# Kernel optimization log

Hardware: AMD Instinct MI355X
Metric: run time of the kernel (lower is better)

## Reference

```python
import jax, jax.numpy as jnp
import numpy as np

L, B, T, D, H, F = 6, 4, 1024, 512, 8, 2048
DH = D // H
BIAS_DIM = 2
E = 65536
EPS = 1e-3  # LayerNormalization default epsilon in the source


def _ln(x, scale, bias):
    m = jnp.mean(x, axis=-1, keepdims=True)
    v = jnp.mean(jnp.square(x - m), axis=-1, keepdims=True)  # tf.nn.moments: population variance
    return (x - m) * jax.lax.rsqrt(v + EPS) * scale + bias


def setup_inputs() -> dict:
    key = jax.random.key(0)
    ks = jax.random.split(key, 24)
    g = lambda k, shape: (jax.random.normal(k, shape, jnp.float32) * (shape[-1] ** -0.5))
    states = jax.random.normal(ks[0], (B, T, D), jnp.float32)
    # causal mask broadcast over heads: [B, 1, Tq, Tk]
    masks = jnp.tril(jnp.ones((T, T), jnp.float32))[None, None] * jnp.ones((B, 1, 1, 1), jnp.float32)
    # sparse bias edges: columns (edge_type, batch_idx, key_idx, query_idx)
    et = jax.random.randint(ks[1], (E, 1), 0, BIAS_DIM)
    bi = jax.random.randint(ks[2], (E, 1), 0, B)
    ki = jax.random.randint(ks[3], (E, 1), 0, T)
    qi = jax.random.randint(ks[4], (E, 1), 0, T)
    attention_bias = jnp.concatenate([et, bi, ki, qi], axis=1).astype(jnp.int32)
    return dict(
        states=states,
        masks=masks,
        attention_bias=attention_bias,
        Wq=g(ks[5], (L, D, H, DH)),
        Wk=g(ks[6], (L, D, H, DH)),
        Wv=g(ks[7], (L, D, H, DH)),
        Wo=g(ks[8], (L, H, DH, D)),
        Eb=g(ks[9], (L, BIAS_DIM, DH)),
        Es=g(ks[10], (L, DH)),
        ln1_s=jnp.ones((L, D), jnp.float32),
        ln1_b=jnp.zeros((L, D), jnp.float32),
        ln2_s=jnp.ones((L, D), jnp.float32),
        ln2_b=jnp.zeros((L, D), jnp.float32),
        lno_s=jnp.ones((D,), jnp.float32),
        lno_b=jnp.zeros((D,), jnp.float32),
        W1=g(ks[11], (L, D, F)),
        b1=jnp.zeros((L, F), jnp.float32),
        W2=g(ks[12], (L, F, D)),
        b2=jnp.zeros((L, D), jnp.float32),
    )


def reference(states, masks, attention_bias, Wq, Wk, Wv, Wo, Eb, Es,
              ln1_s, ln1_b, ln2_s, ln2_b, lno_s, lno_b, W1, b1, W2, b2):
    FMIN = jnp.finfo(jnp.float32).min
    scale = jnp.float32(DH) ** -0.5
    et, bi, ki, qi = (attention_bias[:, 0], attention_bias[:, 1],
                      attention_bias[:, 2], attention_bias[:, 3])
    for l in range(L):
        # --- self-attention with edge bias ---
        x = _ln(states, ln1_s[l], ln1_b[l])
        q = jnp.einsum('btd,dha->btha', x, Wq[l])
        k = jnp.einsum('btd,dha->btha', x, Wk[l])
        v = jnp.einsum('btd,dha->btha', x, Wv[l])
        alpha = jnp.einsum('bkha,bqha->bhqk', k, q)
        # edge-type embedding -> scalar per edge, scatter into dense [B,q,k] (duplicates sum)
        bias_val = Eb[l][et] @ Es[l]  # [E]
        bias3 = jnp.zeros((B, T, T), jnp.float32).at[bi, ki, qi].add(bias_val)
        alpha = alpha + jnp.einsum('bqk,bkh->bhqk', bias3, k.sum(-1))
        alpha = alpha * scale
        alpha = alpha * masks + (1.0 - jnp.ceil(masks)) * FMIN
        alpha = jax.nn.softmax(alpha, axis=-1) * masks  # mask-softmax-renormalize (no renorm, just re-mask)
        ctx = jnp.einsum('bhqk,bkha->bqha', alpha, v)
        states = states + jnp.einsum('btha,had->btd', ctx, Wo[l])
        # --- FFN ---
        h = jax.nn.relu(_ln(states, ln2_s[l], ln2_b[l]) @ W1[l] + b1[l])
        states = states + h @ W2[l] + b2[l]
    return _ln(states, lno_s, lno_b)
```

## Files before the change

kernel.cpp:

```cpp
#include <hip/hip_runtime.h>
#include <hip/hip_bf16.h>
#include <cstdint>

#define LNUM 6
#define BNUM 4
#define TSEQ 1024
#define DMOD 512
#define HNUM 8
#define FDIM 2048
#define DHEAD 64
#define NEVENTS 65536
#define EPS_LN 1e-3f
#define ATT_SCALE 0.125f

#define GF_ACC 1
#define GF_RELU 2
#define GF_BIAS 4
#define GF_SPLIT 8
#define GF_QKV 16
#define GF_PART 32

typedef float f32x4 __attribute__((ext_vector_type(4)));
typedef short bf16x8 __attribute__((ext_vector_type(8)));
typedef unsigned short u16;
typedef unsigned int u32;

__device__ inline u16 f2bf(float f){
  u32 u = __builtin_bit_cast(u32, f);
  u32 r = (u + 0x7fffu + ((u >> 16) & 1u)) >> 16;
  return (u16)r;
}
__device__ inline float bf2f(u16 u){
  return __builtin_bit_cast(float, (u32)u << 16);
}
__device__ inline void split2(float x, u16 &hi, u16 &lo){
  u16 h = f2bf(x);
  lo = f2bf(x - bf2f(h));
  hi = h;
}
__device__ inline void gload16(const void* g, void* l){
  __builtin_amdgcn_global_load_lds(
      (const __attribute__((address_space(1))) void*)g,
      (__attribute__((address_space(3))) void*)l, 16, 0, 0);
}

__global__ __launch_bounds__(256) void ln_kernel(float* __restrict__ x,
    const float* __restrict__ part, const float* __restrict__ abias,
    const float* __restrict__ s, const float* __restrict__ bsh,
    float* __restrict__ yf, u16* __restrict__ yh, u16* __restrict__ yl, int mode){
  int row = blockIdx.x, tid = threadIdx.x;
  float* xr = x + (size_t)row * DMOD;
  float2 v = *reinterpret_cast<const float2*>(xr + tid*2);
  if (part){
    const size_t MN = (size_t)BNUM*TSEQ*DMOD;
    const size_t o = (size_t)row*DMOD + tid*2;
    float2 p0 = *reinterpret_cast<const float2*>(part + o);
    float2 p1 = *reinterpret_cast<const float2*>(part + MN + o);
    v.x += p0.x + p1.x; v.y += p0.y + p1.y;
    if (abias){
      v.x += abias[tid*2]; v.y += abias[tid*2+1];
    }
    *reinterpret_cast<float2*>(xr + tid*2) = v;
  }
  float sum = v.x + v.y, sq = v.x*v.x + v.y*v.y;
  #pragma unroll
  for (int off = 32; off > 0; off >>= 1){
    sum += __shfl_down(sum, off);
    sq  += __shfl_down(sq, off);
  }
  __shared__ float ss[4], sq2[4];
  int wid = tid >> 6;
  if ((tid & 63) == 0){ ss[wid] = sum; sq2[wid] = sq; }
  __syncthreads();
  sum = ss[0]+ss[1]+ss[2]+ss[3];
  sq  = sq2[0]+sq2[1]+sq2[2]+sq2[3];
  float mean = sum * (1.f/DMOD);
  float var  = sq * (1.f/DMOD) - mean*mean;
  float rstd = rsqrtf(var + EPS_LN);
  float2 sc = *reinterpret_cast<const float2*>(s + tid*2);
  float2 bi = *reinterpret_cast<const float2*>(bsh + tid*2);
  float ox = (v.x - mean)*rstd*sc.x + bi.x;
  float oy = (v.y - mean)*rstd*sc.y + bi.y;
  if (mode == 0){
    u16 h0,l0,h1,l1;
    split2(ox,h0,l0); split2(oy,h1,l1);
    *(u32*)(yh + (size_t)row*DMOD + tid*2) = (u32)h0 | ((u32)h1<<16);
    *(u32*)(yl + (size_t)row*DMOD + tid*2) = (u32)l0 | ((u32)l1<<16);
  } else {
    float2 o; o.x = ox; o.y = oy;
    *reinterpret_cast<float2*>(yf + (size_t)row*DMOD + tid*2) = o;
  }
}

__global__ __launch_bounds__(256) void wsplit5(
    const float* __restrict__ Wq, const float* __restrict__ Wk,
    const float* __restrict__ Wv, const float* __restrict__ Wo,
    const float* __restrict__ W1, int l,
    u16* __restrict__ wqkvh, u16* __restrict__ wqkvl,
    u16* __restrict__ woh,   u16* __restrict__ wol,
    u16* __restrict__ w1h,   u16* __restrict__ w1l){
  __shared__ float T[64][65];
  int id = blockIdx.x;
  const float* src; u16 *dh, *dl; int N, bx, by;
  if (id < 256){
    const int which = id >> 6, sub = id & 63;
    bx = sub & 7; by = sub >> 3; N = 512;
    if (which == 0){ src = Wq; dh = wqkvh;            dl = wqkvl; }
    else if (which == 1){ src = Wk; dh = wqkvh + 512*512; dl = wqkvl + 512*512; }
    else if (which == 2){ src = Wv; dh = wqkvh + 2*512*512; dl = wqkvl + 2*512*512; }
    else { src = Wo; dh = woh; dl = wol; }
    src += (size_t)l*DMOD*DMOD;
  } else {
    id -= 256;
    bx = id & 31; by = id >> 5; N = 2048;
    src = W1 + (size_t)l*DMOD*FDIM; dh = w1h; dl = w1l;
  }
  const int k0 = by*64, n0 = bx*64;
  const int tid = threadIdx.x;
  {
    const int r = tid>>2, cseg = (tid&3)*16;
    const float* sp = src + (size_t)(k0+r)*N + n0 + cseg;
    #pragma unroll
    for (int i = 0; i < 16; i += 4){
      float4 v = *(const float4*)(sp + i);
      T[cseg+i+0][r] = v.x; T[cseg+i+1][r] = v.y;
      T[cseg+i+2][r] = v.z; T[cseg+i+3][r] = v.w;
    }
  }
  __syncthreads();
  const int n = tid>>2, kseg = (tid&3)*16;
  u32 wh[8], wl[8];
  #pragma unroll
  for (int i = 0; i < 8; ++i){
    u16 h0,l0,h1,l1;
    split2(T[n][kseg+2*i], h0, l0);
    split2(T[n][kseg+2*i+1], h1, l1);
    wh[i] = (u32)h0 | ((u32)h1<<16);
    wl[i] = (u32)l0 | ((u32)l1<<16);
  }
  u16* ph = dh + (size_t)(n0+n)*DMOD + k0 + kseg;
  u16* pl = dl + (size_t)(n0+n)*DMOD + k0 + kseg;
  *(uint4*)(ph)   = make_uint4(wh[0],wh[1],wh[2],wh[3]);
  *(uint4*)(ph+8) = make_uint4(wh[4],wh[5],wh[6],wh[7]);
  *(uint4*)(pl)   = make_uint4(wl[0],wl[1],wl[2],wl[3]);
  *(uint4*)(pl+8) = make_uint4(wl[4],wl[5],wl[6],wl[7]);
}

__global__ __launch_bounds__(256) void wsplit(const float* __restrict__ W,
    u16* __restrict__ Thi, u16* __restrict__ Tlo, int K, int N){
  __shared__ float T[64][65];
  const int k0 = blockIdx.y*64, n0 = blockIdx.x*64;
  const int tid = threadIdx.x;
  {
    const int r = tid>>2, cseg = (tid&3)*16;
    const float* src = W + (size_t)(k0+r)*N + n0 + cseg;
    #pragma unroll
    for (int i = 0; i < 16; i += 4){
      float4 v = *(const float4*)(src + i);
      T[cseg+i+0][r] = v.x; T[cseg+i+1][r] = v.y;
      T[cseg+i+2][r] = v.z; T[cseg+i+3][r] = v.w;
    }
  }
  __syncthreads();
  const int n = tid>>2, kseg = (tid&3)*16;
  u32 wh[8], wl[8];
  #pragma unroll
  for (int i = 0; i < 8; ++i){
    u16 h0,l0,h1,l1;
    split2(T[n][kseg+2*i], h0, l0);
    split2(T[n][kseg+2*i+1], h1, l1);
    wh[i] = (u32)h0 | ((u32)h1<<16);
    wl[i] = (u32)l0 | ((u32)l1<<16);
  }
  u16* dh = Thi + (size_t)(n0+n)*K + k0 + kseg;
  u16* dl = Tlo + (size_t)(n0+n)*K + k0 + kseg;
  *(uint4*)(dh)   = make_uint4(wh[0],wh[1],wh[2],wh[3]);
  *(uint4*)(dh+8) = make_uint4(wh[4],wh[5],wh[6],wh[7]);
  *(uint4*)(dl)   = make_uint4(wl[0],wl[1],wl[2],wl[3]);
  *(uint4*)(dl+8) = make_uint4(wl[4],wl[5],wl[6],wl[7]);
}

template<int BN, int NS, int FLAGS>
__global__ __launch_bounds__(256) void gemm_mfma(
    const u16* __restrict__ Ahi, const u16* __restrict__ Alo,
    const u16* __restrict__ Bhi, const u16* __restrict__ Blo,
    const float* __restrict__ bias, float* __restrict__ C,
    u16* __restrict__ Ohi, u16* __restrict__ Olo,
    u16* __restrict__ Vhi, u16* __restrict__ Vlo,
    int M, int N, int K, int kc){
  constexpr int NA  = 16;
  constexpr int NB  = BN/8;
  constexpr int PER = (NA+NB)/4;
  __shared__ __align__(16) unsigned char As[128*128];
  __shared__ __align__(16) unsigned char Bs[BN*128];
  const int tid = threadIdx.x, wid = tid>>6, lane = tid&63;
  const int li = lane&15, g = lane>>4;
  const int nxb = N/BN;
  const int cpx = gridDim.x >> 3;
  const int bid = blockIdx.x;
  const int wg  = (bid&7)*cpx + (bid>>3);
  const int bx = wg % nxb, by = wg / nxb;
  const int m0 = by*128, n0 = bx*BN;
  const int wr = wid>>1, wc = wid&1;
  const int kbeg = blockIdx.y * kc, kend = kbeg + kc;
  f32x4 acc[4][NS] = {};

  for (int k0 = kbeg; k0 < kend; k0 += 32){
    __syncthreads();
    #pragma unroll
    for (int i = 0; i < PER; ++i){
      const int issue = wid*PER + i;
      const bool isA = issue < NA;
      const int ia = isA ? issue : issue - NA;
      const int c = ia*64 + lane;
      const int row = c>>3, slot = c&7;
      const int sg = slot ^ (row&7);
      const u16* base = isA ? (sg < 4 ? Ahi : Alo) : (sg < 4 ? Bhi : Blo);
      const int gr = (isA ? m0 : n0) + row;
      const u16* gp = base + (size_t)gr*K + k0 + (sg&3)*8;
      unsigned char* lp = (isA ? As : Bs) + ia*1024 + lane*16;
      gload16(gp, lp);
    }
    __syncthreads();
    bf16x8 ah[4], al[4], bh[NS], bl[NS];
    #pragma unroll
    for (int ms = 0; ms < 4; ++ms){
      const int r = wr*64 + ms*16 + li; const int x = (r&7)<<4;
      const unsigned char* p = As + r*128;
      ah[ms] = *(const bf16x8*)(p + ((g*16)^x));
      al[ms] = *(const bf16x8*)(p + ((64 + g*16)^x));
    }
    #pragma unroll
    for (int ns = 0; ns < NS; ++ns){
      const int r = wc*(BN/2) + ns*16 + li; const int x = (r&7)<<4;
      const unsigned char* p = Bs + r*128;
      bh[ns] = *(const bf16x8*)(p + ((g*16)^x));
      bl[ns] = *(const bf16x8*)(p + ((64 + g*16)^x));
    }
    #pragma unroll
    for (int ms = 0; ms < 4; ++ms)
      #pragma unroll
      for (int ns = 0; ns < NS; ++ns){
        acc[ms][ns] = __builtin_amdgcn_mfma_f32_16x16x32_bf16(ah[ms], bh[ns], acc[ms][ns], 0, 0, 0);
        acc[ms][ns] = __builtin_amdgcn_mfma_f32_16x16x32_bf16(ah[ms], bl[ns], acc[ms][ns], 0, 0, 0);
        acc[ms][ns] = __builtin_amdgcn_mfma_f32_16x16x32_bf16(al[ms], bh[ns], acc[ms][ns], 0, 0, 0);
      }
  }
  #pragma unroll
  for (int ms = 0; ms < 4; ++ms){
    #pragma unroll
    for (int ns = 0; ns < NS; ++ns){
      #pragma unroll
      for (int r = 0; r < 4; ++r){
        const int m = m0 + wr*64 + ms*16 + g*4 + r;
        const int n = n0 + wc*(BN/2) + ns*16 + li;
        float val = acc[ms][ns][r];
        if (FLAGS & GF_BIAS) val += bias[n];
        if (FLAGS & GF_RELU) val = fmaxf(val, 0.f);
        if (FLAGS & GF_QKV){
          u16 vh, vl; split2(val, vh, vl);
          if (n < 1024){
            const size_t ix = (size_t)m*1024 + n;
            Ohi[ix] = vh; Olo[ix] = vl;
          } else {
            const size_t ix = ((size_t)(m>>10)*DMOD + (n-1024))*TSEQ + (m&1023);
            Vhi[ix] = vh; Vlo[ix] = vl;
          }
        } else if (FLAGS & GF_SPLIT){
          u16 vh, vl; split2(val, vh, vl);
          const size_t ix = (size_t)m*N + n;
          Ohi[ix] = vh; Olo[ix] = vl;
        } else if (FLAGS & GF_PART){
          C[(size_t)blockIdx.y*M*N + (size_t)m*N + n] = val;
        } else {
          const size_t ix = (size_t)m*N + n;
          if (FLAGS & GF_ACC) val += C[ix];
          C[ix] = val;
        }
      }
    }
  }
}

__global__ __launch_bounds__(256) void ksum_kernel(const u16* __restrict__ kh_,
    const u16* __restrict__ kl_, float* __restrict__ ks){
  int idx = blockIdx.x*256 + threadIdx.x;
  const size_t base = (size_t)(idx>>3)*1024 + 512 + (idx&7)*DHEAD;
  const u16* ph = kh_ + base;
  const u16* pl = kl_ + base;
  float s = 0.f;
  #pragma unroll
  for (int a = 0; a < DHEAD; a += 8){
    bf16x8 vh = *(const bf16x8*)(ph + a);
    bf16x8 vl = *(const bf16x8*)(pl + a);
    #pragma unroll
    for (int j = 0; j < 8; ++j) s += bf2f((u16)vh[j]) + bf2f((u16)vl[j]);
  }
  ks[idx] = s;
}

__global__ __launch_bounds__(256) void scatter_kernel(const int* __restrict__ ab,
    const float* __restrict__ Eb, const float* __restrict__ Es, float* __restrict__ bias3){
  __shared__ float d2[2];
  if (threadIdx.x < 2){
    float v = 0.f;
    #pragma unroll
    for (int a = 0; a < DHEAD; ++a) v += Eb[threadIdx.x*DHEAD + a]*Es[a];
    d2[threadIdx.x] = v;
  }
  __syncthreads();
  int e = blockIdx.x*256 + threadIdx.x;
  int4 r = *reinterpret_cast<const int4*>(ab + (size_t)e*4);
  atomicAdd(bias3 + ((size_t)r.y*TSEQ + r.z)*TSEQ + r.w, d2[r.x]);
}

__device__ __forceinline__ void tile_compute(
    const unsigned char* __restrict__ Klh, const unsigned char* __restrict__ Kll,
    const unsigned char* __restrict__ Vh, const unsigned char* __restrict__ Vl,
    unsigned char* __restrict__ Plh, unsigned char* __restrict__ Pll,
    const float* __restrict__ ksl, const float* __restrict__ bb,
    int kt, int rowg0, int wid, int li, int g,
    const bf16x8* qah, const bf16x8* qal,
    f32x4* oacc, float* mrun, float* srun){
  f32x4 sacc[4] = {};
  #pragma unroll
  for (int jb = 0; jb < 4; ++jb){
    const int rb = (jb*16 + li)*128, x = (li & 7) << 4;
    #pragma unroll
    for (int k2 = 0; k2 < 2; ++k2){
      bf16x8 kfh = *(const bf16x8*)(Klh + rb + ((g*16 + k2*64)^x));
      bf16x8 kfl = *(const bf16x8*)(Kll + rb + ((g*16 + k2*64)^x));
      sacc[jb] = __builtin_amdgcn_mfma_f32_16x16x32_bf16(qah[k2], kfh, sacc[jb], 0, 0, 0);
      sacc[jb] = __builtin_amdgcn_mfma_f32_16x16x32_bf16(qah[k2], kfl, sacc[jb], 0, 0, 0);
      sacc[jb] = __builtin_amdgcn_mfma_f32_16x16x32_bf16(qal[k2], kfh, sacc[jb], 0, 0, 0);
    }
  }
  #pragma unroll
  for (int jb = 0; jb < 4; ++jb){
    const int colg = kt + jb*16 + li;
    const float ksv = ksl[jb*16 + li];
    #pragma unroll
    for (int r = 0; r < 4; ++r){
      const int rowg = rowg0 + r;
      float s = (sacc[jb][r] + bb[(size_t)rowg*TSEQ + colg] * ksv) * ATT_SCALE;
      sacc[jb][r] = (colg <= rowg) ? s : -INFINITY;
    }
  }
  #pragma unroll
  for (int r = 0; r < 4; ++r){
    float tm = fmaxf(fmaxf(sacc[0][r], sacc[1][r]), fmaxf(sacc[2][r], sacc[3][r]));
    tm = fmaxf(tm, __shfl_xor(tm, 1));
    tm = fmaxf(tm, __shfl_xor(tm, 2));
    tm = fmaxf(tm, __shfl_xor(tm, 4));
    tm = fmaxf(tm, __shfl_xor(tm, 8));
    const float nm = fmaxf(mrun[r], tm);
    const float fac = __expf(mrun[r] - nm);
    mrun[r] = nm;
    float p0 = __expf(sacc[0][r] - nm);
    float p1 = __expf(sacc[1][r] - nm);
    float p2 = __expf(sacc[2][r] - nm);
    float p3 = __expf(sacc[3][r] - nm);
    float rs = p0 + p1 + p2 + p3;
    rs += __shfl_xor(rs, 1);
    rs += __shfl_xor(rs, 2);
    rs += __shfl_xor(rs, 4);
    rs += __shfl_xor(rs, 8);
    srun[r] = srun[r]*fac + rs;
    oacc[0][r] *= fac; oacc[1][r] *= fac; oacc[2][r] *= fac; oacc[3][r] *= fac;
    const int prow = g*4 + r;
    const int pb = wid*2048 + prow*128, px = (prow & 7) << 4;
    u16 ph0,pl0, ph1,pl1, ph2,pl2, ph3,pl3;
    split2(p0,ph0,pl0); split2(p1,ph1,pl1); split2(p2,ph2,pl2); split2(p3,ph3,pl3);
    *(u16*)(Plh + pb + ((li*2 +  0)^px)) = ph0;
    *(u16*)(Plh + pb + ((li*2 + 32)^px)) = ph1;
    *(u16*)(Plh + pb + ((li*2 + 64)^px)) = ph2;
    *(u16*)(Plh + pb + ((li*2 + 96)^px)) = ph3;
    *(u16*)(Pll + pb + ((li*2 +  0)^px)) = pl0;
    *(u16*)(Pll + pb + ((li*2 + 32)^px)) = pl1;
    *(u16*)(Pll + pb + ((li*2 + 64)^px)) = pl2;
    *(u16*)(Pll + pb + ((li*2 + 96)^px)) = pl3;
  }
  bf16x8 pah[2], pal[2];
  {
    const int pb = wid*2048 + li*128, x = (li & 7) << 4;
    pah[0] = *(const bf16x8*)(Plh + pb + ((g*16     )^x));
    pah[1] = *(const bf16x8*)(Plh + pb + ((g*16 + 64)^x));
    pal[0] = *(const bf16x8*)(Pll + pb + ((g*16     )^x));
    pal[1] = *(const bf16x8*)(Pll + pb + ((g*16 + 64)^x));
  }
  #pragma unroll
  for (int ja = 0; ja < 4; ++ja){
    const int vb = (ja*16 + li)*128, x = (li & 7) << 4;
    #pragma unroll
    for (int k2 = 0; k2 < 2; ++k2){
      bf16x8 vfh = *(const bf16x8*)(Vh + vb + ((g*16 + k2*64)^x));
      bf16x8 vfl = *(const bf16x8*)(Vl + vb + ((g*16 + k2*64)^x));
      oacc[ja] = __builtin_amdgcn_mfma_f32_16x16x32_bf16(pah[k2], vfh, oacc[ja], 0, 0, 0);
      oacc[ja] = __builtin_amdgcn_mfma_f32_16x16x32_bf16(pah[k2], vfl, oacc[ja], 0, 0, 0);
      oacc[ja] = __builtin_amdgcn_mfma_f32_16x16x32_bf16(pal[k2], vfh, oacc[ja], 0, 0, 0);
    }
  }
}

__global__ __launch_bounds__(256) void attn_split(
    const u16* __restrict__ qkh, const u16* __restrict__ qkl,
    const u16* __restrict__ vth, const u16* __restrict__ vtl,
    const float* __restrict__ ksum, const float* __restrict__ bias3,
    u16* __restrict__ ch_, u16* __restrict__ cl_){
  __shared__ __align__(16) unsigned char Klh[8192], Kll[8192], Vh[8192], Vl[8192];
  __shared__ __align__(16) unsigned char Plh[8192], Pll[8192];
  __shared__ float ksl[64];

  const int bid = blockIdx.x;
  const int p = bid & 7, h = (bid >> 3) & 7, b = bid >> 6;
  const int qA0 = p*64, qB0 = (15-p)*64;
  const int tid = threadIdx.x, wid = tid >> 6, lane = tid & 63;
  const int li = lane & 15, g = lane >> 4;
  const int rowA0 = qA0 + wid*16 + g*4;
  const int rowB0 = qB0 + wid*16 + g*4;

  bf16x8 qahA[2], qalA[2], qahB[2], qalB[2];
  {
    const size_t offA = (size_t)(b*TSEQ + qA0 + wid*16 + li)*1024 + h*DHEAD;
    const size_t offB = (size_t)(b*TSEQ + qB0 + wid*16 + li)*1024 + h*DHEAD;
    #pragma unroll
    for (int k2 = 0; k2 < 2; ++k2){
      qahA[k2] = *(const bf16x8*)(qkh + offA + g*8 + k2*32);
      qalA[k2] = *(const bf16x8*)(qkl + offA + g*8 + k2*32);
      qahB[k2] = *(const bf16x8*)(qkh + offB + g*8 + k2*32);
      qalB[k2] = *(const bf16x8*)(qkl + offB + g*8 + k2*32);
    }
  }

  f32x4 oaccA[4] = {}, oaccB[4] = {};
  float mrunA[4] = {-INFINITY,-INFINITY,-INFINITY,-INFINITY};
  float mrunB[4] = {-INFINITY,-INFINITY,-INFINITY,-INFINITY};
  float srunA[4] = {0.f,0.f,0.f,0.f};
  float srunB[4] = {0.f,0.f,0.f,0.f};

  const int krow = tid >> 2, part = tid & 3;
  const int lbase = krow*128, lx = (krow & 7) << 4;
  const float* bb = bias3 + (size_t)b*TSEQ*TSEQ;

  uint4 rk0, rk1, rk2, rk3, rv0, rv1, rv2, rv3;
  float ksr = 0.f;
  auto issue = [&](int kt){
    const size_t koff = (size_t)(b*TSEQ + kt + krow)*1024 + 512 + h*DHEAD + part*16;
    rk0 = *(const uint4*)(qkh + koff);
    rk1 = *(const uint4*)(qkh + koff + 8);
    rk2 = *(const uint4*)(qkl + koff);
    rk3 = *(const uint4*)(qkl + koff + 8);
    const size_t voff = ((size_t)b*DMOD + h*DHEAD + krow)*TSEQ + kt + part*16;
    rv0 = *(const uint4*)(vth + voff);
    rv1 = *(const uint4*)(vth + voff + 8);
    rv2 = *(const uint4*)(vtl + voff);
    rv3 = *(const uint4*)(vtl + voff + 8);
    if (tid < 64) ksr = ksum[(size_t)(b*TSEQ + kt + tid)*HNUM + h];
  };

  issue(0);
  for (int kt = 0; kt <= qB0; kt += 64){
    *(uint4*)(Klh + lbase + ((part*32     )^lx)) = rk0;
    *(uint4*)(Klh + lbase + ((part*32 + 16)^lx)) = rk1;
    *(uint4*)(Kll + lbase + ((part*32     )^lx)) = rk2;
    *(uint4*)(Kll + lbase + ((part*32 + 16)^lx)) = rk3;
    *(uint4*)(Vh  + lbase + ((part*32     )^lx)) = rv0;
    *(uint4*)(Vh  + lbase + ((part*32 + 16)^lx)) = rv1;
    *(uint4*)(Vl  + lbase + ((part*32     )^lx)) = rv2;
    *(uint4*)(Vl  + lbase + ((part*32 + 16)^lx)) = rv3;
    if (tid < 64) ksl[tid] = ksr;
    __syncthreads();
    if (kt + 64 <= qB0) issue(kt + 64);
    tile_compute(Klh, Kll, Vh, Vl, Plh, Pll, ksl, bb, kt, rowB0, wid, li, g,
                 qahB, qalB, oaccB, mrunB, srunB);
    if (kt <= qA0)
      tile_compute(Klh, Kll, Vh, Vl, Plh, Pll, ksl, bb, kt, rowA0, wid, li, g,
                   qahA, qalA, oaccA, mrunA, srunA);
    __syncthreads();
  }

  #pragma unroll
  for (int ja = 0; ja < 4; ++ja){
    #pragma unroll
    for (int r = 0; r < 4; ++r){
      {
        const float val = oaccB[ja][r] / srunB[r];
        u16 vh, vl; split2(val, vh, vl);
        const size_t ix = (size_t)(b*TSEQ + rowB0 + r)*DMOD + h*DHEAD + ja*16 + li;
        ch_[ix] = vh; cl_[ix] = vl;
      }
      {
        const float val = oaccA[ja][r] / srunA[r];
        u16 vh, vl; split2(val, vh, vl);
        const size_t ix = (size_t)(b*TSEQ + rowA0 + r)*DMOD + h*DHEAD + ja*16 + li;
        ch_[ix] = vh; cl_[ix] = vl;
      }
    }
  }
}

extern "C" void kernel_launch(void* const* d_in, const int* in_sizes, int n_in,
                              void* d_out, int out_size, void* d_ws, size_t ws_size,
                              hipStream_t stream){
  const float* states0 = (const float*)d_in[0];
  const int*   ab      = (const int*)d_in[2];
  const float* Wq = (const float*)d_in[3];
  const float* Wk = (const float*)d_in[4];
  const float* Wv = (const float*)d_in[5];
  const float* Wo = (const float*)d_in[6];
  const float* Eb = (const float*)d_in[7];
  const float* Es = (const float*)d_in[8];
  const float* ln1_s = (const float*)d_in[9];
  const float* ln1_b = (const float*)d_in[10];
  const float* ln2_s = (const float*)d_in[11];
  const float* ln2_b = (const float*)d_in[12];
  const float* lno_s = (const float*)d_in[13];
  const float* lno_b = (const float*)d_in[14];
  const float* W1 = (const float*)d_in[15];
  const float* b1 = (const float*)d_in[16];
  const float* W2 = (const float*)d_in[17];
  const float* b2 = (const float*)d_in[18];
  float* out = (float*)d_out;

  char* ws = (char*)d_ws;
  const size_t MB = 1024*1024;
  float* states = (float*)(ws);
  u16* xh  = (u16*)(ws + 8*MB);
  u16* xl  = (u16*)(ws + 12*MB);
  u16* qkh = (u16*)(ws + 16*MB);
  u16* qkl = (u16*)(ws + 24*MB);
  u16* vth = (u16*)(ws + 32*MB);
  u16* vtl = (u16*)(ws + 36*MB);
  u16* cth = (u16*)(ws + 40*MB);
  u16* ctl = (u16*)(ws + 44*MB);
  float* ksum  = (float*)(ws + 48*MB);
  float* bias3 = (float*)(ws + 48*MB + 131072);
  char*  wA    = ws + 64*MB + 131072;
  char*  wB    = wA + 4*MB;
  u16* hh = qkh;
  u16* hl = vth;
  float* part = bias3;

  u16* wqkvh = (u16*)(wA);
  u16* wqkvl = (u16*)(wA + 1536*1024);
  u16* woh   = (u16*)(wA + 3*MB);
  u16* wol   = (u16*)(wA + 3*MB + 512*1024);
  u16* w2h   = (u16*)(wA);
  u16* w2l   = (u16*)(wA + 2*MB);
  u16* w1h   = (u16*)(wB);
  u16* w1l   = (u16*)(wB + 2*MB);

  hipMemcpyAsync(states, states0, 8*MB, hipMemcpyDeviceToDevice, stream);

  const int NROW = BNUM*TSEQ;
  dim3 blk(256);
  for (int l = 0; l < LNUM; ++l){
    wsplit5<<<512, blk, 0, stream>>>(Wq, Wk, Wv, Wo, W1, l,
        wqkvh, wqkvl, woh, wol, w1h, w1l);

    ln_kernel<<<NROW, blk, 0, stream>>>(states,
        (l == 0) ? nullptr : part, (l == 0) ? nullptr : b2 + (size_t)(l-1)*DMOD,
        ln1_s + l*DMOD, ln1_b + l*DMOD, nullptr, xh, xl, 0);
    gemm_mfma<128,4, GF_SPLIT|GF_QKV><<<384, blk, 0, stream>>>(
        xh, xl, wqkvh, wqkvl, nullptr, nullptr, qkh, qkl, vth, vtl, NROW, 1536, DMOD, DMOD);
    ksum_kernel<<<(BNUM*TSEQ*HNUM)/256, blk, 0, stream>>>(qkh, qkl, ksum);
    hipMemsetAsync(bias3, 0, (size_t)BNUM*TSEQ*TSEQ*sizeof(float), stream);
    scatter_kernel<<<NEVENTS/256, blk, 0, stream>>>(ab, Eb + (size_t)l*2*DHEAD, Es + (size_t)l*DHEAD, bias3);
    attn_split<<<BNUM*HNUM*8, blk, 0, stream>>>(qkh, qkl, vth, vtl, ksum, bias3, cth, ctl);
    gemm_mfma<64,2, GF_PART><<<dim3(256,2), blk, 0, stream>>>(
        cth, ctl, woh, wol, nullptr, part, nullptr, nullptr, nullptr, nullptr, NROW, DMOD, DMOD, DMOD/2);

    wsplit<<<dim3(8,32), blk, 0, stream>>>(W2 + (size_t)l*FDIM*DMOD, w2h, w2l, FDIM, DMOD);
    ln_kernel<<<NROW, blk, 0, stream>>>(states, part, nullptr,
        ln2_s + l*DMOD, ln2_b + l*DMOD, nullptr, xh, xl, 0);
    gemm_mfma<128,4, GF_BIAS|GF_RELU|GF_SPLIT><<<512, blk, 0, stream>>>(
        xh, xl, w1h, w1l, b1 + (size_t)l*FDIM, nullptr, hh, hl, nullptr, nullptr, NROW, FDIM, DMOD, DMOD);
    gemm_mfma<64,2, GF_PART><<<dim3(256,2), blk, 0, stream>>>(
        hh, hl, w2h, w2l, nullptr, part, nullptr, nullptr, nullptr, nullptr, NROW, DMOD, FDIM, FDIM/2);
  }
  ln_kernel<<<NROW, blk, 0, stream>>>(states, part, b2 + (size_t)(LNUM-1)*DMOD,
      lno_s, lno_b, out, nullptr, nullptr, 1);
}
```

Measured before the change: 1.309 ms.

## Split attention key tiles across two blocks and merge partial softmax results

The attention kernel now launches twice as many blocks. Each block processes alternating (even or odd) key tiles and writes unnormalized partial outputs plus per-row max and sum statistics. A new merge kernel combines the two partials with log-sum-exp rescaling. This aims to raise parallelism, since the old grid had only 256 blocks, at the cost of extra partial-output traffic, a second launch, and a split-bf16 round-trip of the unnormalized accumulators. The output buffer and the xh/xl buffers are reused as scratch.

```diff
diff --git a/kernel.cpp b/kernel.cpp
--- a/kernel.cpp
+++ b/kernel.cpp
@@ -406,18 +406,25 @@
     const u16* __restrict__ qkh, const u16* __restrict__ qkl,
     const u16* __restrict__ vth, const u16* __restrict__ vtl,
     const float* __restrict__ ksum, const float* __restrict__ bias3,
-    u16* __restrict__ ch_, u16* __restrict__ cl_){
+    u16* __restrict__ o0h, u16* __restrict__ o0l,
+    u16* __restrict__ o1h, u16* __restrict__ o1l,
+    float* __restrict__ mst){
   __shared__ __align__(16) unsigned char Klh[8192], Kll[8192], Vh[8192], Vl[8192];
   __shared__ __align__(16) unsigned char Plh[8192], Pll[8192];
   __shared__ float ksl[64];
 
   const int bid = blockIdx.x;
-  const int p = bid & 7, h = (bid >> 3) & 7, b = bid >> 6;
+  const int parity = bid & 1, p = (bid >> 1) & 7, h = (bid >> 4) & 7, b = bid >> 7;
   const int qA0 = p*64, qB0 = (15-p)*64;
   const int tid = threadIdx.x, wid = tid >> 6, lane = tid & 63;
   const int li = lane & 15, g = lane >> 4;
   const int rowA0 = qA0 + wid*16 + g*4;
   const int rowB0 = qB0 + wid*16 + g*4;
+  const int NBt = 16 - p, NAt = p + 1;
+
+  u16* oh = parity ? o1h : o0h;
+  u16* ol = parity ? o1l : o0l;
+  float* ms = mst + parity*65536;
 
   bf16x8 qahA[2], qalA[2], qahB[2], qalB[2];
   {
@@ -458,8 +465,9 @@
     if (tid < 64) ksr = ksum[(size_t)(b*TSEQ + kt + tid)*HNUM + h];
   };
 
-  issue(0);
-  for (int kt = 0; kt <= qB0; kt += 64){
+  issue(parity*64);
+  for (int idx = parity; idx < NBt; idx += 2){
+    const int kt = idx*64;
     *(uint4*)(Klh + lbase + ((part*32     )^lx)) = rk0;
     *(uint4*)(Klh + lbase + ((part*32 + 16)^lx)) = rk1;
     *(uint4*)(Kll + lbase + ((part*32     )^lx)) = rk2;
@@ -470,33 +478,73 @@
     *(uint4*)(Vl  + lbase + ((part*32 + 16)^lx)) = rv3;
     if (tid < 64) ksl[tid] = ksr;
     __syncthreads();
-    if (kt + 64 <= qB0) issue(kt + 64);
+    if (idx + 2 < NBt) issue((idx + 2)*64);
     tile_compute(Klh, Kll, Vh, Vl, Plh, Pll, ksl, bb, kt, rowB0, wid, li, g,
                  qahB, qalB, oaccB, mrunB, srunB);
-    if (kt <= qA0)
+    if (idx < NAt)
       tile_compute(Klh, Kll, Vh, Vl, Plh, Pll, ksl, bb, kt, rowA0, wid, li, g,
                    qahA, qalA, oaccA, mrunA, srunA);
     __syncthreads();
   }
 
   #pragma unroll
-  for (int ja = 0; ja < 4; ++ja){
-    #pragma unroll
-    for (int r = 0; r < 4; ++r){
+  for (int r = 0; r < 4; ++r){
+    if (li == 0){
+      const size_t rixB = ((size_t)(b*TSEQ + rowB0 + r)*HNUM + h);
+      ms[rixB*2 + 0] = mrunB[r];
+      ms[rixB*2 + 1] = srunB[r];
+      const size_t rixA = ((size_t)(b*TSEQ + rowA0 + r)*HNUM + h);
+      ms[rixA*2 + 0] = mrunA[r];
+      ms[rixA*2 + 1] = srunA[r];
+    }
+    #pragma unroll
+    for (int ja = 0; ja < 4; ++ja){
       {
-        const float val = oaccB[ja][r] / srunB[r];
-        u16 vh, vl; split2(val, vh, vl);
+        u16 vh, vl; split2(oaccB[ja][r], vh, vl);
         const size_t ix = (size_t)(b*TSEQ + rowB0 + r)*DMOD + h*DHEAD + ja*16 + li;
-        ch_[ix] = vh; cl_[ix] = vl;
+        oh[ix] = vh; ol[ix] = vl;
       }
       {
-        const float val = oaccA[ja][r] / srunA[r];
-        u16 vh, vl; split2(val, vh, vl);
+        u16 vh, vl; split2(oaccA[ja][r], vh, vl);
         const size_t ix = (size_t)(b*TSEQ + rowA0 + r)*DMOD + h*DHEAD + ja*16 + li;
-        ch_[ix] = vh; cl_[ix] = vl;
+        oh[ix] = vh; ol[ix] = vl;
       }
     }
   }
+}
+
+__global__ __launch_bounds__(256) void attn_merge(
+    const u16* __restrict__ o0h, const u16* __restrict__ o0l,
+    const u16* __restrict__ o1h, const u16* __restrict__ o1l,
+    const float* __restrict__ mst, u16* __restrict__ ch_, u16* __restrict__ cl_){
+  const size_t base = ((size_t)blockIdx.x*256 + threadIdx.x)*2;
+  const int bt = (int)(base >> 9), col = (int)(base & 511);
+  const int h = col >> 6;
+  const size_t rix = (size_t)bt*HNUM + h;
+  const float m0 = mst[rix*2], s0 = mst[rix*2 + 1];
+  const float m1 = mst[65536 + rix*2], s1 = mst[65536 + rix*2 + 1];
+  float m = -INFINITY;
+  if (s0 > 0.f) m = m0;
+  if (s1 > 0.f) m = fmaxf(m, m1);
+  const float f0 = (s0 > 0.f) ? __expf(m0 - m) : 0.f;
+  const float f1 = (s1 > 0.f) ? __expf(m1 - m) : 0.f;
+  const float sinv = 1.f / (s0*f0 + s1*f1);
+  const u32 a0h = *(const u32*)(o0h + base);
+  const u32 a0l = *(const u32*)(o0l + base);
+  const u32 a1h = *(const u32*)(o1h + base);
+  const u32 a1l = *(const u32*)(o1l + base);
+  u32 outh = 0, outl = 0;
+  #pragma unroll
+  for (int j = 0; j < 2; ++j){
+    const float o0 = bf2f((u16)(a0h >> (16*j))) + bf2f((u16)(a0l >> (16*j)));
+    const float o1 = bf2f((u16)(a1h >> (16*j))) + bf2f((u16)(a1l >> (16*j)));
+    const float val = (o0*f0 + o1*f1) * sinv;
+    u16 vh, vl; split2(val, vh, vl);
+    outh |= (u32)vh << (16*j);
+    outl |= (u32)vl << (16*j);
+  }
+  *(u32*)(ch_ + base) = outh;
+  *(u32*)(cl_ + base) = outl;
 }
 
 extern "C" void kernel_launch(void* const* d_in, const int* in_sizes, int n_in,
@@ -540,6 +588,7 @@
   u16* hh = qkh;
   u16* hl = vth;
   float* part = bias3;
+  float* mst  = out;
 
   u16* wqkvh = (u16*)(wA);
   u16* wqkvl = (u16*)(wA + 1536*1024);
@@ -566,7 +615,9 @@
     ksum_kernel<<<(BNUM*TSEQ*HNUM)/256, blk, 0, stream>>>(qkh, qkl, ksum);
     hipMemsetAsync(bias3, 0, (size_t)BNUM*TSEQ*TSEQ*sizeof(float), stream);
     scatter_kernel<<<NEVENTS/256, blk, 0, stream>>>(ab, Eb + (size_t)l*2*DHEAD, Es + (size_t)l*DHEAD, bias3);
-    attn_split<<<BNUM*HNUM*8, blk, 0, stream>>>(qkh, qkl, vth, vtl, ksum, bias3, cth, ctl);
+    attn_split<<<BNUM*HNUM*8*2, blk, 0, stream>>>(qkh, qkl, vth, vtl, ksum, bias3,
+        cth, ctl, xh, xl, mst);
+    attn_merge<<<(NROW*DMOD)/512, blk, 0, stream>>>(cth, ctl, xh, xl, mst, cth, ctl);
     gemm_mfma<64,2, GF_PART><<<dim3(256,2), blk, 0, stream>>>(
         cth, ctl, woh, wol, nullptr, part, nullptr, nullptr, nullptr, nullptr, NROW, DMOD, DMOD, DMOD/2);
 
```

New measurement: 1.356 ms. +3.6%, slower.

## Split attention query tiles across two wave groups in a 512-thread block

Applied to the files above, without the earlier changes.

The attention kernel now launches 512 threads per block. Two groups of four waves each own one of the paired query tiles (the short causal one and the long one) and share the staged K/V tiles, where before the same four waves processed both tiles one after the other. The per-wave P scratch is doubled, and each thread stages one 16-byte chunk per K/V buffer instead of two. This doubles the waves per CU for latency hiding and runs the two tiles concurrently. The cost is that the short-tile group sits idle through the later iterations, and register and LDS pressure rise under launch_bounds(512,1).

```diff
diff --git a/kernel.cpp b/kernel.cpp
--- a/kernel.cpp
+++ b/kernel.cpp
@@ -402,80 +402,69 @@
   }
 }
 
-__global__ __launch_bounds__(256) void attn_split(
+__global__ __launch_bounds__(512, 1) void attn_split(
     const u16* __restrict__ qkh, const u16* __restrict__ qkl,
     const u16* __restrict__ vth, const u16* __restrict__ vtl,
     const float* __restrict__ ksum, const float* __restrict__ bias3,
     u16* __restrict__ ch_, u16* __restrict__ cl_){
   __shared__ __align__(16) unsigned char Klh[8192], Kll[8192], Vh[8192], Vl[8192];
-  __shared__ __align__(16) unsigned char Plh[8192], Pll[8192];
+  __shared__ __align__(16) unsigned char Plh[16384], Pll[16384];
   __shared__ float ksl[64];
 
   const int bid = blockIdx.x;
   const int p = bid & 7, h = (bid >> 3) & 7, b = bid >> 6;
-  const int qA0 = p*64, qB0 = (15-p)*64;
   const int tid = threadIdx.x, wid = tid >> 6, lane = tid & 63;
+  const int grp = wid >> 2, wid4 = wid & 3;
   const int li = lane & 15, g = lane >> 4;
-  const int rowA0 = qA0 + wid*16 + g*4;
-  const int rowB0 = qB0 + wid*16 + g*4;
-
-  bf16x8 qahA[2], qalA[2], qahB[2], qalB[2];
+  const int q0 = grp ? (15-p)*64 : p*64;
+  const int NT = grp ? (16-p) : (p+1);
+  const int NB = 16 - p;
+  const int row0 = q0 + wid4*16 + g*4;
+
+  bf16x8 qah[2], qal[2];
   {
-    const size_t offA = (size_t)(b*TSEQ + qA0 + wid*16 + li)*1024 + h*DHEAD;
-    const size_t offB = (size_t)(b*TSEQ + qB0 + wid*16 + li)*1024 + h*DHEAD;
+    const size_t off = (size_t)(b*TSEQ + q0 + wid4*16 + li)*1024 + h*DHEAD;
     #pragma unroll
     for (int k2 = 0; k2 < 2; ++k2){
-      qahA[k2] = *(const bf16x8*)(qkh + offA + g*8 + k2*32);
-      qalA[k2] = *(const bf16x8*)(qkl + offA + g*8 + k2*32);
-      qahB[k2] = *(const bf16x8*)(qkh + offB + g*8 + k2*32);
-      qalB[k2] = *(const bf16x8*)(qkl + offB + g*8 + k2*32);
-    }
-  }
-
-  f32x4 oaccA[4] = {}, oaccB[4] = {};
-  float mrunA[4] = {-INFINITY,-INFINITY,-INFINITY,-INFINITY};
-  float mrunB[4] = {-INFINITY,-INFINITY,-INFINITY,-INFINITY};
-  float srunA[4] = {0.f,0.f,0.f,0.f};
-  float srunB[4] = {0.f,0.f,0.f,0.f};
-
-  const int krow = tid >> 2, part = tid & 3;
+      qah[k2] = *(const bf16x8*)(qkh + off + g*8 + k2*32);
+      qal[k2] = *(const bf16x8*)(qkl + off + g*8 + k2*32);
+    }
+  }
+
+  f32x4 oacc[4] = {};
+  float mrun[4] = {-INFINITY,-INFINITY,-INFINITY,-INFINITY};
+  float srun[4] = {0.f,0.f,0.f,0.f};
+
+  const int krow = tid >> 3, part8 = tid & 7;
   const int lbase = krow*128, lx = (krow & 7) << 4;
+  const int lslot = (part8*16) ^ lx;
   const float* bb = bias3 + (size_t)b*TSEQ*TSEQ;
 
-  uint4 rk0, rk1, rk2, rk3, rv0, rv1, rv2, rv3;
+  uint4 rkh, rkl, rvh, rvl;
   float ksr = 0.f;
   auto issue = [&](int kt){
-    const size_t koff = (size_t)(b*TSEQ + kt + krow)*1024 + 512 + h*DHEAD + part*16;
-    rk0 = *(const uint4*)(qkh + koff);
-    rk1 = *(const uint4*)(qkh + koff + 8);
-    rk2 = *(const uint4*)(qkl + koff);
-    rk3 = *(const uint4*)(qkl + koff + 8);
-    const size_t voff = ((size_t)b*DMOD + h*DHEAD + krow)*TSEQ + kt + part*16;
-    rv0 = *(const uint4*)(vth + voff);
-    rv1 = *(const uint4*)(vth + voff + 8);
-    rv2 = *(const uint4*)(vtl + voff);
-    rv3 = *(const uint4*)(vtl + voff + 8);
+    const size_t koff = (size_t)(b*TSEQ + kt + krow)*1024 + 512 + h*DHEAD + part8*8;
+    rkh = *(const uint4*)(qkh + koff);
+    rkl = *(const uint4*)(qkl + koff);
+    const size_t voff = ((size_t)b*DMOD + h*DHEAD + krow)*TSEQ + kt + part8*8;
+    rvh = *(const uint4*)(vth + voff);
+    rvl = *(const uint4*)(vtl + voff);
     if (tid < 64) ksr = ksum[(size_t)(b*TSEQ + kt + tid)*HNUM + h];
   };
 
   issue(0);
-  for (int kt = 0; kt <= qB0; kt += 64){
-    *(uint4*)(Klh + lbase + ((part*32     )^lx)) = rk0;
-    *(uint4*)(Klh + lbase + ((part*32 + 16)^lx)) = rk1;
-    *(uint4*)(Kll + lbase + ((part*32     )^lx)) = rk2;
-    *(uint4*)(Kll + lbase + ((part*32 + 16)^lx)) = rk3;
-    *(uint4*)(Vh  + lbase + ((part*32     )^lx)) = rv0;
-    *(uint4*)(Vh  + lbase + ((part*32 + 16)^lx)) = rv1;
-    *(uint4*)(Vl  + lbase + ((part*32     )^lx)) = rv2;
-    *(uint4*)(Vl  + lbase + ((part*32 + 16)^lx)) = rv3;
+  for (int it = 0; it < NB; ++it){
+    const int kt = it*64;
+    *(uint4*)(Klh + lbase + lslot) = rkh;
+    *(uint4*)(Kll + lbase + lslot) = rkl;
+    *(uint4*)(Vh  + lbase + lslot) = rvh;
+    *(uint4*)(Vl  + lbase + lslot) = rvl;
     if (tid < 64) ksl[tid] = ksr;
     __syncthreads();
-    if (kt + 64 <= qB0) issue(kt + 64);
-    tile_compute(Klh, Kll, Vh, Vl, Plh, Pll, ksl, bb, kt, rowB0, wid, li, g,
-                 qahB, qalB, oaccB, mrunB, srunB);
-    if (kt <= qA0)
-      tile_compute(Klh, Kll, Vh, Vl, Plh, Pll, ksl, bb, kt, rowA0, wid, li, g,
-                   qahA, qalA, oaccA, mrunA, srunA);
+    if (it + 1 < NB) issue(kt + 64);
+    if (it < NT)
+      tile_compute(Klh, Kll, Vh, Vl, Plh, Pll, ksl, bb, kt, row0, wid, li, g,
+                   qah, qal, oacc, mrun, srun);
     __syncthreads();
   }
 
@@ -483,18 +472,10 @@
   for (int ja = 0; ja < 4; ++ja){
     #pragma unroll
     for (int r = 0; r < 4; ++r){
-      {
-        const float val = oaccB[ja][r] / srunB[r];
-        u16 vh, vl; split2(val, vh, vl);
-        const size_t ix = (size_t)(b*TSEQ + rowB0 + r)*DMOD + h*DHEAD + ja*16 + li;
-        ch_[ix] = vh; cl_[ix] = vl;
-      }
-      {
-        const float val = oaccA[ja][r] / srunA[r];
-        u16 vh, vl; split2(val, vh, vl);
-        const size_t ix = (size_t)(b*TSEQ + rowA0 + r)*DMOD + h*DHEAD + ja*16 + li;
-        ch_[ix] = vh; cl_[ix] = vl;
-      }
+      const float val = oacc[ja][r] / srun[r];
+      u16 vh, vl; split2(val, vh, vl);
+      const size_t ix = (size_t)(b*TSEQ + row0 + r)*DMOD + h*DHEAD + ja*16 + li;
+      ch_[ix] = vh; cl_[ix] = vl;
     }
   }
 }
@@ -566,7 +547,7 @@
     ksum_kernel<<<(BNUM*TSEQ*HNUM)/256, blk, 0, stream>>>(qkh, qkl, ksum);
     hipMemsetAsync(bias3, 0, (size_t)BNUM*TSEQ*TSEQ*sizeof(float), stream);
     scatter_kernel<<<NEVENTS/256, blk, 0, stream>>>(ab, Eb + (size_t)l*2*DHEAD, Es + (size_t)l*DHEAD, bias3);
-    attn_split<<<BNUM*HNUM*8, blk, 0, stream>>>(qkh, qkl, vth, vtl, ksum, bias3, cth, ctl);
+    attn_split<<<BNUM*HNUM*8, dim3(512), 0, stream>>>(qkh, qkl, vth, vtl, ksum, bias3, cth, ctl);
     gemm_mfma<64,2, GF_PART><<<dim3(256,2), blk, 0, stream>>>(
         cth, ctl, woh, wol, nullptr, part, nullptr, nullptr, nullptr, nullptr, NROW, DMOD, DMOD, DMOD/2);
 
```

Result: slower. 1.487 ms (+13.6%).

## Scatter edge-type counts once and rebuild bias per layer inside attention

Applied to the files above, without the earlier changes.

The per-layer dense fp32 bias scatter (memset plus atomic scatter of 16MB) is replaced by a single up-front scatter that counts edges per cell and edge type into packed 8-bit counters in a u16 grid held in the output buffer. The attention kernel computes the two per-type scalars from Eb and Es and reconstructs the bias as count0*d0 + count1*d1, reading 2 bytes per cell instead of 4. This removes six memset/scatter passes and halves bias bandwidth in attention. It risks 8-bit counter overflow if many duplicate edges land on one cell, and it reuses the output buffer as scratch until the final layernorm overwrites it.

```diff
diff --git a/kernel.cpp b/kernel.cpp
--- a/kernel.cpp
+++ b/kernel.cpp
@@ -299,26 +299,21 @@
   ks[idx] = s;
 }
 
-__global__ __launch_bounds__(256) void scatter_kernel(const int* __restrict__ ab,
-    const float* __restrict__ Eb, const float* __restrict__ Es, float* __restrict__ bias3){
-  __shared__ float d2[2];
-  if (threadIdx.x < 2){
-    float v = 0.f;
-    #pragma unroll
-    for (int a = 0; a < DHEAD; ++a) v += Eb[threadIdx.x*DHEAD + a]*Es[a];
-    d2[threadIdx.x] = v;
-  }
-  __syncthreads();
+__global__ __launch_bounds__(256) void scatter_cnt(const int* __restrict__ ab,
+    u32* __restrict__ cntw){
   int e = blockIdx.x*256 + threadIdx.x;
   int4 r = *reinterpret_cast<const int4*>(ab + (size_t)e*4);
-  atomicAdd(bias3 + ((size_t)r.y*TSEQ + r.z)*TSEQ + r.w, d2[r.x]);
+  const size_t cell = ((size_t)r.y*TSEQ + r.z)*TSEQ + r.w;
+  const u32 inc = (r.x ? 0x100u : 1u) << (16*(cell & 1));
+  atomicAdd(cntw + (cell >> 1), inc);
 }
 
 __device__ __forceinline__ void tile_compute(
     const unsigned char* __restrict__ Klh, const unsigned char* __restrict__ Kll,
     const unsigned char* __restrict__ Vh, const unsigned char* __restrict__ Vl,
     unsigned char* __restrict__ Plh, unsigned char* __restrict__ Pll,
-    const float* __restrict__ ksl, const float* __restrict__ bb,
+    const float* __restrict__ ksl, const u16* __restrict__ bb,
+    float d0, float d1,
     int kt, int rowg0, int wid, int li, int g,
     const bf16x8* qah, const bf16x8* qal,
     f32x4* oacc, float* mrun, float* srun){
@@ -342,7 +337,9 @@
     #pragma unroll
     for (int r = 0; r < 4; ++r){
       const int rowg = rowg0 + r;
-      float s = (sacc[jb][r] + bb[(size_t)rowg*TSEQ + colg] * ksv) * ATT_SCALE;
+      const u32 c = bb[(size_t)rowg*TSEQ + colg];
+      const float bv = (float)(c & 0xff)*d0 + (float)(c >> 8)*d1;
+      float s = (sacc[jb][r] + bv * ksv) * ATT_SCALE;
       sacc[jb][r] = (colg <= rowg) ? s : -INFINITY;
     }
   }
@@ -405,7 +402,8 @@
 __global__ __launch_bounds__(256) void attn_split(
     const u16* __restrict__ qkh, const u16* __restrict__ qkl,
     const u16* __restrict__ vth, const u16* __restrict__ vtl,
-    const float* __restrict__ ksum, const float* __restrict__ bias3,
+    const float* __restrict__ ksum, const u16* __restrict__ cnt,
+    const float* __restrict__ Ebl, const float* __restrict__ Esl,
     u16* __restrict__ ch_, u16* __restrict__ cl_){
   __shared__ __align__(16) unsigned char Klh[8192], Kll[8192], Vh[8192], Vl[8192];
   __shared__ __align__(16) unsigned char Plh[8192], Pll[8192];
@@ -419,6 +417,14 @@
   const int rowA0 = qA0 + wid*16 + g*4;
   const int rowB0 = qB0 + wid*16 + g*4;
 
+  float d0 = 0.f, d1 = 0.f;
+  #pragma unroll 8
+  for (int a = 0; a < DHEAD; ++a){
+    const float e = Esl[a];
+    d0 += Ebl[a] * e;
+    d1 += Ebl[DHEAD + a] * e;
+  }
+
   bf16x8 qahA[2], qalA[2], qahB[2], qalB[2];
   {
     const size_t offA = (size_t)(b*TSEQ + qA0 + wid*16 + li)*1024 + h*DHEAD;
@@ -440,7 +446,7 @@
 
   const int krow = tid >> 2, part = tid & 3;
   const int lbase = krow*128, lx = (krow & 7) << 4;
-  const float* bb = bias3 + (size_t)b*TSEQ*TSEQ;
+  const u16* bb = cnt + (size_t)b*TSEQ*TSEQ;
 
   uint4 rk0, rk1, rk2, rk3, rv0, rv1, rv2, rv3;
   float ksr = 0.f;
@@ -471,10 +477,10 @@
     if (tid < 64) ksl[tid] = ksr;
     __syncthreads();
     if (kt + 64 <= qB0) issue(kt + 64);
-    tile_compute(Klh, Kll, Vh, Vl, Plh, Pll, ksl, bb, kt, rowB0, wid, li, g,
+    tile_compute(Klh, Kll, Vh, Vl, Plh, Pll, ksl, bb, d0, d1, kt, rowB0, wid, li, g,
                  qahB, qalB, oaccB, mrunB, srunB);
     if (kt <= qA0)
-      tile_compute(Klh, Kll, Vh, Vl, Plh, Pll, ksl, bb, kt, rowA0, wid, li, g,
+      tile_compute(Klh, Kll, Vh, Vl, Plh, Pll, ksl, bb, d0, d1, kt, rowA0, wid, li, g,
                    qahA, qalA, oaccA, mrunA, srunA);
     __syncthreads();
   }
@@ -534,12 +540,12 @@
   u16* cth = (u16*)(ws + 40*MB);
   u16* ctl = (u16*)(ws + 44*MB);
   float* ksum  = (float*)(ws + 48*MB);
-  float* bias3 = (float*)(ws + 48*MB + 131072);
+  float* part  = (float*)(ws + 48*MB + 131072);
   char*  wA    = ws + 64*MB + 131072;
   char*  wB    = wA + 4*MB;
   u16* hh = qkh;
   u16* hl = vth;
-  float* part = bias3;
+  u16* cnt = (u16*)d_out;
 
   u16* wqkvh = (u16*)(wA);
   u16* wqkvl = (u16*)(wA + 1536*1024);
@@ -551,6 +557,8 @@
   u16* w1l   = (u16*)(wB + 2*MB);
 
   hipMemcpyAsync(states, states0, 8*MB, hipMemcpyDeviceToDevice, stream);
+  hipMemsetAsync(d_out, 0, (size_t)BNUM*TSEQ*TSEQ*sizeof(u16), stream);
+  scatter_cnt<<<NEVENTS/256, 256, 0, stream>>>(ab, (u32*)d_out);
 
   const int NROW = BNUM*TSEQ;
   dim3 blk(256);
@@ -564,9 +572,8 @@
     gemm_mfma<128,4, GF_SPLIT|GF_QKV><<<384, blk, 0, stream>>>(
         xh, xl, wqkvh, wqkvl, nullptr, nullptr, qkh, qkl, vth, vtl, NROW, 1536, DMOD, DMOD);
     ksum_kernel<<<(BNUM*TSEQ*HNUM)/256, blk, 0, stream>>>(qkh, qkl, ksum);
-    hipMemsetAsync(bias3, 0, (size_t)BNUM*TSEQ*TSEQ*sizeof(float), stream);
-    scatter_kernel<<<NEVENTS/256, blk, 0, stream>>>(ab, Eb + (size_t)l*2*DHEAD, Es + (size_t)l*DHEAD, bias3);
-    attn_split<<<BNUM*HNUM*8, blk, 0, stream>>>(qkh, qkl, vth, vtl, ksum, bias3, cth, ctl);
+    attn_split<<<BNUM*HNUM*8, blk, 0, stream>>>(qkh, qkl, vth, vtl, ksum, cnt,
+        Eb + (size_t)l*2*DHEAD, Es + (size_t)l*DHEAD, cth, ctl);
     gemm_mfma<64,2, GF_PART><<<dim3(256,2), blk, 0, stream>>>(
         cth, ctl, woh, wol, nullptr, part, nullptr, nullptr, nullptr, nullptr, NROW, DMOD, DMOD, DMOD/2);
 
```

Result: faster. 1.279 ms (-2.3%).
